# Kernel tuning notes

Hardware: AMD Instinct MI355X
Metric: run time of the kernel (lower is better)

## Reference

```python
import jax, jax.numpy as jnp
import numpy as np
import math

B, S, H, NH = 2, 2048, 2048, 16
HD = H // NH
LAYER_NUMBER = 5
NORM_FACTOR = math.sqrt(HD) * LAYER_NUMBER  # sqrt(head_dim) * coeff
BETA = 1.0 / LAYER_NUMBER
SCALE = float(LAYER_NUMBER)  # ScaledSoftmax scale = coeff
MASK_VALUE = -10000.0


def setup_inputs() -> dict:
    key = jax.random.key(0)
    ks = jax.random.split(key, 6)
    inv_sqrt_h = 1.0 / math.sqrt(H)
    return {
        "hidden_states": jax.random.normal(ks[0], (B, S, H), jnp.float32),
        "alibi": jax.random.normal(ks[1], (NH, 1, S), jnp.float32) * 0.1,
        "w_qkv": jax.random.normal(ks[2], (3 * H, H), jnp.float32) * inv_sqrt_h,
        "b_qkv": jax.random.normal(ks[3], (3 * H,), jnp.float32) * 0.02,
        "w_dense": jax.random.normal(ks[4], (H, H), jnp.float32) * inv_sqrt_h,
        "b_dense": jax.random.normal(ks[5], (H,), jnp.float32) * 0.02,
        "attention_mask": jnp.ones((B, S), jnp.int32),
    }


def reference(hidden_states, alibi, w_qkv, b_qkv, w_dense, b_dense, attention_mask):
    b, s, h = hidden_states.shape
    # QKV projection: [b, s, 3h] -> [b, s, nh, 3*hd] -> split
    mixed = hidden_states @ w_qkv.T + b_qkv
    mixed = mixed.reshape(b, s, NH, 3 * HD)
    q, k, v = jnp.split(mixed, 3, axis=-1)  # each [b, s, nh, hd]

    # Faithful Megatron-style memory reinterpretation (row-major reshape),
    # exactly matching torch's .contiguous().view(s, b*nh, hd).
    q2 = jnp.swapaxes(q.reshape(s, b * NH, HD), 0, 1)  # [b*nh, q_len, hd]
    k2 = jnp.swapaxes(k.reshape(s, b * NH, HD), 0, 1)  # [b*nh, k_len, hd]
    v2 = jnp.swapaxes(v.reshape(s, b * NH, HD), 0, 1)  # [b*nh, k_len, hd]

    # baddbmm: alibi*beta + (q @ k^T)/norm_factor
    alibi_b = jnp.tile(alibi, (b, 1, 1))[: b * NH, :, :s]  # [b*nh, 1, k_len]
    scores = alibi_b * BETA + jnp.einsum("bqd,bkd->bqk", q2, k2) * (1.0 / NORM_FACTOR)
    scores = scores.reshape(b, NH, s, s)

    # ScaledSoftmax: scale then fused causal+padding mask fill, then softmax
    scores = scores * SCALE
    pad_bool = (1 - attention_mask).astype(bool)  # True where padded
    causal = jnp.tril(jnp.ones((s, s), dtype=bool))
    bad = pad_bool[:, None, :, None] | (~causal)[None, None, :, :]  # [b,1,s,s]
    scores = jnp.where(bad, MASK_VALUE, scores)
    probs = jax.nn.softmax(scores, axis=-1)  # [b, nh, s, s]

    # context = probs @ V with the same faithful reshapes
    probs_r = probs.reshape(b * NH, s, s)
    context = jnp.einsum("bqk,bkd->bqd", probs_r, v2)  # [b*nh, q_len, hd]
    context = context.reshape(b, NH, s, HD)
    context = jnp.transpose(context, (2, 0, 1, 3)).reshape(s, b, h)  # [s, b, h]

    out = context @ w_dense.T + b_dense  # [s, b, h]
    return jnp.swapaxes(out, 0, 1)  # [b, s, h]
```

## Files before the change

### kernel.cpp

```cpp
#include <hip/hip_runtime.h>

typedef unsigned short u16;
typedef __bf16  bf16x8 __attribute__((ext_vector_type(8)));
typedef float   f32x4  __attribute__((ext_vector_type(4)));
typedef u16     u16x8  __attribute__((ext_vector_type(8)));
typedef u16     u16x4  __attribute__((ext_vector_type(4)));

#define QSCALE 0.12751744545f

__device__ __forceinline__ u16 f2b(float f) {
    unsigned u = __float_as_uint(f);
    unsigned r = u + 0x7FFFu + ((u >> 16) & 1u);
    return (u16)(r >> 16);
}
__device__ __forceinline__ float b2f(u16 b) {
    return __uint_as_float(((unsigned)b) << 16);
}
__device__ __forceinline__ void async16(const u16* g, u16* l) {
    __builtin_amdgcn_global_load_lds(
        (__attribute__((address_space(1))) void*)(u16*)g,
        (__attribute__((address_space(3))) void*)l, 16, 0, 0);
}

__global__ void cvt_f32_bf16(const float* __restrict__ in, u16* __restrict__ out, int n4) {
    int i = blockIdx.x * blockDim.x + threadIdx.x;
    if (i >= n4) return;
    float4 f = ((const float4*)in)[i];
    u16x4 o;
    o[0] = f2b(f.x); o[1] = f2b(f.y); o[2] = f2b(f.z); o[3] = f2b(f.w);
    *(u16x4*)(out + (size_t)i * 4) = o;
}

__global__ void cvt_wqkv(const float* __restrict__ in, u16* __restrict__ out, int n4) {
    int i = blockIdx.x * blockDim.x + threadIdx.x;
    if (i >= n4) return;
    int row = i >> 9;
    float s = ((row % 384) < 128) ? QSCALE : 1.0f;
    float4 f = ((const float4*)in)[i];
    u16x4 o;
    o[0] = f2b(f.x * s); o[1] = f2b(f.y * s); o[2] = f2b(f.z * s); o[3] = f2b(f.w * s);
    *(u16x4*)(out + (size_t)i * 4) = o;
}

__global__ __launch_bounds__(512, 2) void gemm_qkv(
    const u16* __restrict__ A, const u16* __restrict__ B,
    const float* __restrict__ bias,
    u16* __restrict__ qb, u16* __restrict__ kb, u16* __restrict__ vb)
{
    constexpr int K  = 2048;
    constexpr int NS = K / 32;
    __shared__ u16 lds[65536];

    const int tid = threadIdx.x, wave = tid >> 6, lane = tid & 63;
    const int lm = lane & 15, lg = lane >> 4;
    const int wr = wave >> 2, wc = wave & 3;

    const int rbase = blockIdx.y * 256;
    const int cbase = blockIdx.x * 256;

    const int srl = lane >> 2;
    const int scs = ((lane & 3) ^ ((lane >> 3) & 3)) << 3;
    const u16* sl0;
    int lbase;
    {
        int qq = (wave & 3) * 4;
        if (wave < 4) { sl0 = A + (size_t)rbase * K; lbase = qq * 512; }
        else          { sl0 = B + (size_t)cbase * K; lbase = 8192 + qq * 512; }
        sl0 += (size_t)(qq * 16 + srl) * K + scs;
    }
    auto stage2 = [&](int s_, int c0) {
        int slot = (s_ & 3) * 16384;
        size_t k0 = (size_t)s_ * 32;
        for (int c = c0; c < c0 + 2; c++)
            async16(sl0 + (size_t)c * 16 * K + k0, &lds[slot + lbase + c * 512]);
    };

    const int coff = (lg ^ ((lm >> 1) & 3)) << 3;
    const int aoff = (wr * 128 + lm) * 32 + coff;
    const int boff = 8192 + (wc * 64 + lm) * 32 + coff;

    f32x4 acc[8][4];
    for (int m = 0; m < 8; m++)
        for (int n = 0; n < 4; n++)
            acc[m][n] = (f32x4){0.f, 0.f, 0.f, 0.f};

    stage2(0, 0); stage2(0, 2);
    stage2(1, 0); stage2(1, 2);
    stage2(2, 0); stage2(2, 2);
    asm volatile("s_waitcnt vmcnt(8)" ::: "memory");
    __builtin_amdgcn_s_barrier();

    for (int s = 0; s < NS; s++) {
        const u16* sl = &lds[(s & 3) * 16384];
        bf16x8 af[4], bf[4];

        for (int n = 0; n < 4; n++) bf[n] = *(const bf16x8*)&sl[boff + n * 512];
        for (int m = 0; m < 4; m++) af[m] = *(const bf16x8*)&sl[aoff + m * 512];
        if (s + 3 < NS) stage2(s + 3, 0);
        __builtin_amdgcn_s_barrier();
        __builtin_amdgcn_s_setprio(1);
        for (int m = 0; m < 4; m++)
            for (int n = 0; n < 4; n++)
                acc[m][n] = __builtin_amdgcn_mfma_f32_16x16x32_bf16(af[m], bf[n], acc[m][n], 0, 0, 0);
        __builtin_amdgcn_s_setprio(0);
        __builtin_amdgcn_s_barrier();

        for (int m = 0; m < 4; m++) af[m] = *(const bf16x8*)&sl[aoff + (m + 4) * 512];
        if (s + 3 < NS) stage2(s + 3, 2);
        __builtin_amdgcn_s_barrier();
        __builtin_amdgcn_s_setprio(1);
        for (int m = 0; m < 4; m++)
            for (int n = 0; n < 4; n++)
                acc[m + 4][n] = __builtin_amdgcn_mfma_f32_16x16x32_bf16(af[m], bf[n], acc[m + 4][n], 0, 0, 0);
        __builtin_amdgcn_s_setprio(0);

        if (s + 1 < NS) {
            if (s < NS - 3)       asm volatile("s_waitcnt vmcnt(8)" ::: "memory");
            else if (s == NS - 3) asm volatile("s_waitcnt vmcnt(4)" ::: "memory");
            else                  asm volatile("s_waitcnt vmcnt(0)" ::: "memory");
            __builtin_amdgcn_s_barrier();
        }
    }

    __syncthreads();

    const int ct   = (cbase >> 7) + (wc >> 1);
    const int nh   = ct / 3, part = ct - nh * 3;
    const int hd0  = (wc & 1) * 64;
    const int posb = (rbase >> 11) << 10;
    const int sblk = (rbase & 2047) + wr * 128;

    if (part < 2) {
        u16* dst0 = part ? kb : qb;
        const float bsc = part ? 1.0f : QSCALE;
        for (int n = 0; n < 4; n++) {
            int hd = hd0 + n * 16 + lm;
            float bv = bias[ct * 128 + hd] * bsc;
            for (int m = 0; m < 8; m++) {
                for (int r = 0; r < 4; r++) {
                    int s_  = sblk + m * 16 + lg * 4 + r;
                    int bn  = (s_ & 1) * 16 + nh;
                    int pos = posb + (s_ >> 1);
                    dst0[((size_t)(bn * 2048 + pos)) * 128 + hd] = f2b(acc[m][n][r] + bv);
                }
            }
        }
    } else {
        u16* scr = &lds[wave * 8192];
        for (int n = 0; n < 4; n++) {
            int hdl = n * 16 + lm;
            float bv = bias[ct * 128 + hd0 + hdl];
            for (int m = 0; m < 8; m++)
                for (int r = 0; r < 4; r++)
                    scr[(m * 16 + lg * 4 + r) * 64 + hdl] = f2b(acc[m][n][r] + bv);
        }
        int pos0 = posb + (sblk >> 1);
        for (int par = 0; par < 2; par++) {
            int bn = par * 16 + nh;
            u16* dst = vb + ((size_t)(bn * 128 + hd0 + lane)) * 2048 + pos0;
            for (int p8 = 0; p8 < 8; p8++) {
                u16x8 w;
                for (int e = 0; e < 8; e++)
                    w[e] = scr[(2 * (p8 * 8 + e) + par) * 64 + lane];
                *(u16x8*)(dst + p8 * 8) = w;
            }
        }
    }
}

__global__ __launch_bounds__(256) void gemm_bt(
    const u16* __restrict__ A, const u16* __restrict__ B,
    const float* __restrict__ bias, void* __restrict__ C,
    u16* __restrict__ qb, u16* __restrict__ kb, u16* __restrict__ vb,
    int M, int N, int K, int mode)
{
    __shared__ u16 smem[16384];
    u16* As = smem;
    u16* Bs = smem + 8192;

    int tid = threadIdx.x, wave = tid >> 6, lane = tid & 63;
    int lg = lane >> 4, lm = lane & 15;
    int wm = (wave & 1) * 64, wn = (wave >> 1) * 64;

    const u16* Ab = A + (size_t)(blockIdx.y * 128) * K;
    const u16* Bb = B + (size_t)(blockIdx.x * 128) * K;

    f32x4 acc[4][4];
    for (int i = 0; i < 4; i++)
        for (int j = 0; j < 4; j++)
            acc[i][j] = (f32x4){0.f, 0.f, 0.f, 0.f};

    int srow = (lane >> 2), skq = (lane & 3) * 8;

    for (int k0 = 0; k0 < K; k0 += 64) {
        __syncthreads();
        for (int cc = wave; cc < 16; cc += 4) {
            int p = cc >> 3, c = cc & 7;
            int row = c * 16 + srow;
            size_t off = (size_t)row * K + k0 + p * 32 + skq;
            async16(Ab + off, &As[p * 4096 + c * 512]);
            async16(Bb + off, &Bs[p * 4096 + c * 512]);
        }
        __syncthreads();

        for (int p = 0; p < 2; p++) {
            bf16x8 af[4], bf[4];
            for (int i = 0; i < 4; i++) af[i] = *(const bf16x8*)&As[p * 4096 + (wm + i * 16 + lm) * 32 + lg * 8];
            for (int j = 0; j < 4; j++) bf[j] = *(const bf16x8*)&Bs[p * 4096 + (wn + j * 16 + lm) * 32 + lg * 8];
            for (int i = 0; i < 4; i++)
                for (int j = 0; j < 4; j++)
                    acc[i][j] = __builtin_amdgcn_mfma_f32_16x16x32_bf16(af[i], bf[j], acc[i][j], 0, 0, 0);
        }
    }

    if (mode == 1) {
        for (int j = 0; j < 4; j++) {
            int col = blockIdx.x * 128 + wn + j * 16 + lm;
            float bv = bias[col];
            for (int i = 0; i < 4; i++) {
                int row0 = blockIdx.y * 128 + wm + i * 16 + lg * 4;
                for (int r = 0; r < 4; r++) {
                    int row = row0 + r;
                    int orow = ((row & 1) << 11) + (row >> 1);
                    ((float*)C)[(size_t)orow * N + col] = acc[i][j][r] + bv;
                }
            }
        }
        return;
    }

    int ct = blockIdx.x;
    int nh = ct / 3, part = ct - nh * 3;
    float bscale = (part == 0) ? QSCALE : 1.0f;
    int rbase = blockIdx.y * 128;
    int b = rbase >> 11;
    int s0 = rbase & 2047;

    if (part < 2) {
        u16* dst0 = part ? kb : qb;
        for (int j = 0; j < 4; j++) {
            int hd = wn + j * 16 + lm;
            float bv = bias[ct * 128 + hd] * bscale;
            for (int i = 0; i < 4; i++) {
                for (int r = 0; r < 4; r++) {
                    int rl = wm + i * 16 + lg * 4 + r;
                    int s = s0 + rl;
                    int bn = (s & 1) * 16 + nh;
                    int pos = (b << 10) + (s >> 1);
                    dst0[((size_t)(bn * 2048 + pos)) * 128 + hd] = f2b(acc[i][j][r] + bv);
                }
            }
        }
    } else {
        u16 (*arr)[64][128] = (u16(*)[64][128])smem;
        __syncthreads();
        for (int j = 0; j < 4; j++) {
            int hd = wn + j * 16 + lm;
            float bv = bias[ct * 128 + hd];
            for (int i = 0; i < 4; i++) {
                for (int r = 0; r < 4; r++) {
                    int rl = wm + i * 16 + lg * 4 + r;
                    arr[rl & 1][rl >> 1][hd] = f2b(acc[i][j][r] + bv);
                }
            }
        }
        __syncthreads();
        int hd = tid & 127, par = tid >> 7;
        int bn = par * 16 + nh;
        int pos0 = (b << 10) + (s0 >> 1);
        u16* dst = vb + ((size_t)(bn * 128 + hd)) * 2048 + pos0;
        for (int c = 0; c < 8; c++) {
            u16x8 w;
            for (int e = 0; e < 8; e++) w[e] = arr[par][c * 8 + e][hd];
            *(u16x8*)(dst + c * 8) = w;
        }
    }
}

__global__ __launch_bounds__(256) void attn(
    const u16* __restrict__ qb, const u16* __restrict__ kb,
    const u16* __restrict__ vb, const float* __restrict__ alibi,
    u16* __restrict__ ctx)
{
    __shared__ u16 Ks[64 * 136];
    __shared__ u16 Vt[128 * 88];
    __shared__ u16 Ps[4][16 * 72];

    int bn = blockIdx.y;
    int tid = threadIdx.x, wave = tid >> 6, lane = tid & 63;
    int lg = lane >> 4, lm = lane & 15;

    const float* al = alibi + (bn & 15) * 2048;

    int krow = tid >> 2, kq = (tid & 3) * 32;
    int vhd  = tid >> 1, vh2 = (tid & 1) * 32;
    const u16* ksrc0 = kb + (size_t)(bn * 2048 + krow) * 128 + kq;
    const u16* vsrc0 = vb + (size_t)(bn * 128 + vhd) * 2048 + vh2;

    u16* ps = &Ps[wave][0];
    bf16x8 ones;
    {
        u16x8 t;
        for (int j = 0; j < 8; j++) t[j] = 0x3F80;
        ones = *(bf16x8*)&t;
    }

    for (int pass = 0; pass < 2; pass++) {
        int qt = pass ? (31 - blockIdx.x) : blockIdx.x;
        int q0 = qt * 64;

        bf16x8 qf[4];
        {
            const u16* qp = qb + ((size_t)bn * 2048 + q0 + wave * 16 + lm) * 128 + lg * 8;
            for (int kc = 0; kc < 4; kc++) qf[kc] = *(const bf16x8*)(qp + kc * 32);
        }

        f32x4 o[9];
        for (int i = 0; i < 9; i++) o[i] = (f32x4){0.f, 0.f, 0.f, 0.f};

        u16x8 kreg[4], vreg[4];
        for (int i = 0; i < 4; i++) kreg[i] = *(const u16x8*)(ksrc0 + i * 8);
        for (int i = 0; i < 4; i++) vreg[i] = *(const u16x8*)(vsrc0 + i * 8);

        for (int kt = 0; kt <= qt; kt++) {
            int k0 = kt * 64;
            __syncthreads();
            {
                u16* d1 = &Ks[krow * 136 + kq];
                for (int i = 0; i < 4; i++) *(u16x8*)(d1 + i * 8) = kreg[i];
                u16* d2 = &Vt[vhd * 88 + vh2];
                for (int i = 0; i < 4; i++) *(u16x8*)(d2 + i * 8) = vreg[i];
            }
            __syncthreads();

            if (kt < qt) {
                const u16* s1 = ksrc0 + (size_t)(kt + 1) * 64 * 128;
                const u16* s2 = vsrc0 + (kt + 1) * 64;
                for (int i = 0; i < 4; i++) kreg[i] = *(const u16x8*)(s1 + i * 8);
                for (int i = 0; i < 4; i++) vreg[i] = *(const u16x8*)(s2 + i * 8);
            }

            f32x4 sc[4];
            for (int tc = 0; tc < 4; tc++) {
                const u16* kr = &Ks[(tc * 16 + lm) * 136 + lg * 8];
                f32x4 a = (f32x4){0.f, 0.f, 0.f, 0.f};
                for (int kc = 0; kc < 4; kc++)
                    a = __builtin_amdgcn_mfma_f32_16x16x32_bf16(qf[kc], *(const bf16x8*)(kr + kc * 32), a, 0, 0, 0);
                sc[tc] = a;
            }

            bool diag = (kt == qt);
            for (int tc = 0; tc < 4; tc++) {
                int kg = k0 + tc * 16 + lm;
                float av = (al[kg] - 8.0f) * 1.4426950408889634f;
                for (int r = 0; r < 4; r++) {
                    float v = sc[tc][r] + av;
                    if (diag && kg > q0 + wave * 16 + lg * 4 + r) v = -3e38f;
                    ps[(lg * 4 + r) * 72 + tc * 16 + lm] = f2b(__builtin_amdgcn_exp2f(v));
                }
            }

            for (int kc = 0; kc < 2; kc++) {
                bf16x8 pf = *(const bf16x8*)&ps[lm * 72 + kc * 32 + lg * 8];
                for (int i = 0; i < 8; i++) {
                    bf16x8 vf = *(const bf16x8*)&Vt[(i * 16 + lm) * 88 + kc * 32 + lg * 8];
                    o[i] = __builtin_amdgcn_mfma_f32_16x16x32_bf16(pf, vf, o[i], 0, 0, 0);
                }
                o[8] = __builtin_amdgcn_mfma_f32_16x16x32_bf16(pf, ones, o[8], 0, 0, 0);
            }
        }

        for (int r = 0; r < 4; r++) {
            float inv = 1.0f / o[8][r];
            int qg = q0 + wave * 16 + lg * 4 + r;
            int row = qg * 2 + (bn >> 4);
            u16* crow = ctx + (size_t)row * 2048 + (bn & 15) * 128 + lm;
            for (int i = 0; i < 8; i++)
                crow[i * 16] = f2b(o[i][r] * inv);
        }
    }
}

extern "C" void kernel_launch(void* const* d_in, const int* in_sizes, int n_in,
                              void* d_out, int out_size, void* d_ws, size_t ws_size,
                              hipStream_t stream)
{
    const float* hs    = (const float*)d_in[0];
    const float* alibi = (const float*)d_in[1];
    const float* wqkv  = (const float*)d_in[2];
    const float* bqkv  = (const float*)d_in[3];
    const float* wd    = (const float*)d_in[4];
    const float* bd    = (const float*)d_in[5];
    float* out = (float*)d_out;

    char* ws = (char*)d_ws;
    u16* wqkv_b = (u16*)(ws + 0);
    u16* hs_b   = (u16*)(ws + 25165824);
    u16* ctx    = (u16*)(ws + 41943040);
    u16* wd_b   = wqkv_b;
    u16* qb     = (u16*)(ws + 92274688);
    u16* kb     = (u16*)(ws + 109051904);
    u16* vb     = (u16*)(ws + 125829120);

    cvt_f32_bf16<<<8192,  256, 0, stream>>>(hs,   hs_b,   2097152);
    cvt_wqkv   <<<12288, 256, 0, stream>>>(wqkv, wqkv_b, 3145728);

    gemm_qkv<<<dim3(24, 16), 512, 0, stream>>>(hs_b, wqkv_b, bqkv, qb, kb, vb);

    cvt_f32_bf16<<<4096, 256, 0, stream>>>(wd, wd_b, 1048576);

    attn<<<dim3(16, 32), 256, 0, stream>>>(qb, kb, vb, alibi, ctx);

    gemm_bt<<<dim3(16, 32), 256, 0, stream>>>(ctx, wd_b, bd, out,
                                              nullptr, nullptr, nullptr, 4096, 2048, 2048, 1);
}
```

Before: 403.8 us.

## Enlarge attention query tile to 128 rows with XOR-swizzled LDS layout

Each attention workgroup now handles 128 query rows, with every wave computing two 16-row fragments against each K/V tile loaded into LDS. This halves the grid to 8x32 and doubles reuse of each K/V tile. Row padding in the LDS arrays is replaced by an XOR swizzle to avoid bank conflicts. Waves skip key tiles that lie entirely above their causal diagonal. An unused QKV epilogue in the generic GEMM is also deleted. The trade-off is fewer workgroups and more registers per wave, which may reduce occupancy and latency hiding.

New measurement: 411.6 us. No clear change (+1.9%).

```diff
diff --git a/kernel.cpp b/kernel.cpp
--- a/kernel.cpp
+++ b/kernel.cpp
@@ -228,53 +228,6 @@
         }
         return;
     }
-
-    int ct = blockIdx.x;
-    int nh = ct / 3, part = ct - nh * 3;
-    float bscale = (part == 0) ? QSCALE : 1.0f;
-    int rbase = blockIdx.y * 128;
-    int b = rbase >> 11;
-    int s0 = rbase & 2047;
-
-    if (part < 2) {
-        u16* dst0 = part ? kb : qb;
-        for (int j = 0; j < 4; j++) {
-            int hd = wn + j * 16 + lm;
-            float bv = bias[ct * 128 + hd] * bscale;
-            for (int i = 0; i < 4; i++) {
-                for (int r = 0; r < 4; r++) {
-                    int rl = wm + i * 16 + lg * 4 + r;
-                    int s = s0 + rl;
-                    int bn = (s & 1) * 16 + nh;
-                    int pos = (b << 10) + (s >> 1);
-                    dst0[((size_t)(bn * 2048 + pos)) * 128 + hd] = f2b(acc[i][j][r] + bv);
-                }
-            }
-        }
-    } else {
-        u16 (*arr)[64][128] = (u16(*)[64][128])smem;
-        __syncthreads();
-        for (int j = 0; j < 4; j++) {
-            int hd = wn + j * 16 + lm;
-            float bv = bias[ct * 128 + hd];
-            for (int i = 0; i < 4; i++) {
-                for (int r = 0; r < 4; r++) {
-                    int rl = wm + i * 16 + lg * 4 + r;
-                    arr[rl & 1][rl >> 1][hd] = f2b(acc[i][j][r] + bv);
-                }
-            }
-        }
-        __syncthreads();
-        int hd = tid & 127, par = tid >> 7;
-        int bn = par * 16 + nh;
-        int pos0 = (b << 10) + (s0 >> 1);
-        u16* dst = vb + ((size_t)(bn * 128 + hd)) * 2048 + pos0;
-        for (int c = 0; c < 8; c++) {
-            u16x8 w;
-            for (int e = 0; e < 8; e++) w[e] = arr[par][c * 8 + e][hd];
-            *(u16x8*)(dst + c * 8) = w;
-        }
-    }
 }
 
 __global__ __launch_bounds__(256) void attn(
@@ -282,13 +235,14 @@
     const u16* __restrict__ vb, const float* __restrict__ alibi,
     u16* __restrict__ ctx)
 {
-    __shared__ u16 Ks[64 * 136];
-    __shared__ u16 Vt[128 * 88];
-    __shared__ u16 Ps[4][16 * 72];
+    __shared__ u16 Ks[64 * 128];
+    __shared__ u16 Vt[128 * 64];
+    __shared__ u16 Ps[4][32 * 64];
 
     int bn = blockIdx.y;
     int tid = threadIdx.x, wave = tid >> 6, lane = tid & 63;
     int lg = lane >> 4, lm = lane & 15;
+    const int rxor = (lm & 7) * 8;
 
     const float* al = alibi + (bn & 15) * 2048;
 
@@ -296,6 +250,8 @@
     int vhd  = tid >> 1, vh2 = (tid & 1) * 32;
     const u16* ksrc0 = kb + (size_t)(bn * 2048 + krow) * 128 + kq;
     const u16* vsrc0 = vb + (size_t)(bn * 128 + vhd) * 2048 + vh2;
+    const int kxor = (krow & 7) * 8;
+    const int vxor = (vhd & 7) * 8;
 
     u16* ps = &Ps[wave][0];
     bf16x8 ones;
@@ -306,77 +262,98 @@
     }
 
     for (int pass = 0; pass < 2; pass++) {
-        int qt = pass ? (31 - blockIdx.x) : blockIdx.x;
-        int q0 = qt * 64;
-
-        bf16x8 qf[4];
-        {
-            const u16* qp = qb + ((size_t)bn * 2048 + q0 + wave * 16 + lm) * 128 + lg * 8;
-            for (int kc = 0; kc < 4; kc++) qf[kc] = *(const bf16x8*)(qp + kc * 32);
-        }
-
-        f32x4 o[9];
-        for (int i = 0; i < 9; i++) o[i] = (f32x4){0.f, 0.f, 0.f, 0.f};
+        int qtb = pass ? (15 - blockIdx.x) : blockIdx.x;
+        int q0 = qtb * 128;
+        int ktmax = 2 * qtb + 1;
+        int qrow0 = q0 + wave * 32;
+
+        bf16x8 qf[2][4];
+        for (int f = 0; f < 2; f++) {
+            const u16* qp = qb + ((size_t)bn * 2048 + qrow0 + f * 16 + lm) * 128 + lg * 8;
+            for (int kc = 0; kc < 4; kc++) qf[f][kc] = *(const bf16x8*)(qp + kc * 32);
+        }
+
+        f32x4 o[2][9];
+        for (int f = 0; f < 2; f++)
+            for (int i = 0; i < 9; i++) o[f][i] = (f32x4){0.f, 0.f, 0.f, 0.f};
 
         u16x8 kreg[4], vreg[4];
         for (int i = 0; i < 4; i++) kreg[i] = *(const u16x8*)(ksrc0 + i * 8);
         for (int i = 0; i < 4; i++) vreg[i] = *(const u16x8*)(vsrc0 + i * 8);
 
-        for (int kt = 0; kt <= qt; kt++) {
+        for (int kt = 0; kt <= ktmax; kt++) {
             int k0 = kt * 64;
             __syncthreads();
             {
-                u16* d1 = &Ks[krow * 136 + kq];
-                for (int i = 0; i < 4; i++) *(u16x8*)(d1 + i * 8) = kreg[i];
-                u16* d2 = &Vt[vhd * 88 + vh2];
-                for (int i = 0; i < 4; i++) *(u16x8*)(d2 + i * 8) = vreg[i];
+                u16* d1 = &Ks[krow * 128];
+                for (int i = 0; i < 4; i++) *(u16x8*)&d1[(kq + i * 8) ^ kxor] = kreg[i];
+                u16* d2 = &Vt[vhd * 64];
+                for (int i = 0; i < 4; i++) *(u16x8*)&d2[(vh2 + i * 8) ^ vxor] = vreg[i];
             }
             __syncthreads();
 
-            if (kt < qt) {
+            if (kt < ktmax) {
                 const u16* s1 = ksrc0 + (size_t)(kt + 1) * 64 * 128;
                 const u16* s2 = vsrc0 + (kt + 1) * 64;
                 for (int i = 0; i < 4; i++) kreg[i] = *(const u16x8*)(s1 + i * 8);
                 for (int i = 0; i < 4; i++) vreg[i] = *(const u16x8*)(s2 + i * 8);
             }
 
-            f32x4 sc[4];
-            for (int tc = 0; tc < 4; tc++) {
-                const u16* kr = &Ks[(tc * 16 + lm) * 136 + lg * 8];
-                f32x4 a = (f32x4){0.f, 0.f, 0.f, 0.f};
-                for (int kc = 0; kc < 4; kc++)
-                    a = __builtin_amdgcn_mfma_f32_16x16x32_bf16(qf[kc], *(const bf16x8*)(kr + kc * 32), a, 0, 0, 0);
-                sc[tc] = a;
-            }
-
-            bool diag = (kt == qt);
-            for (int tc = 0; tc < 4; tc++) {
-                int kg = k0 + tc * 16 + lm;
-                float av = (al[kg] - 8.0f) * 1.4426950408889634f;
-                for (int r = 0; r < 4; r++) {
-                    float v = sc[tc][r] + av;
-                    if (diag && kg > q0 + wave * 16 + lg * 4 + r) v = -3e38f;
-                    ps[(lg * 4 + r) * 72 + tc * 16 + lm] = f2b(__builtin_amdgcn_exp2f(v));
-                }
-            }
-
-            for (int kc = 0; kc < 2; kc++) {
-                bf16x8 pf = *(const bf16x8*)&ps[lm * 72 + kc * 32 + lg * 8];
-                for (int i = 0; i < 8; i++) {
-                    bf16x8 vf = *(const bf16x8*)&Vt[(i * 16 + lm) * 88 + kc * 32 + lg * 8];
-                    o[i] = __builtin_amdgcn_mfma_f32_16x16x32_bf16(pf, vf, o[i], 0, 0, 0);
-                }
-                o[8] = __builtin_amdgcn_mfma_f32_16x16x32_bf16(pf, ones, o[8], 0, 0, 0);
-            }
-        }
-
-        for (int r = 0; r < 4; r++) {
-            float inv = 1.0f / o[8][r];
-            int qg = q0 + wave * 16 + lg * 4 + r;
-            int row = qg * 2 + (bn >> 4);
-            u16* crow = ctx + (size_t)row * 2048 + (bn & 15) * 128 + lm;
-            for (int i = 0; i < 8; i++)
-                crow[i * 16] = f2b(o[i][r] * inv);
+            bool act = (k0 <= qrow0 + 31);
+            if (act) {
+                f32x4 sc[2][4];
+                for (int tc = 0; tc < 4; tc++) {
+                    const u16* kr = &Ks[(tc * 16 + lm) * 128];
+                    bf16x8 krf[4];
+                    for (int kc = 0; kc < 4; kc++)
+                        krf[kc] = *(const bf16x8*)&kr[(kc * 32 + lg * 8) ^ rxor];
+                    for (int f = 0; f < 2; f++) {
+                        f32x4 a = (f32x4){0.f, 0.f, 0.f, 0.f};
+                        for (int kc = 0; kc < 4; kc++)
+                            a = __builtin_amdgcn_mfma_f32_16x16x32_bf16(qf[f][kc], krf[kc], a, 0, 0, 0);
+                        sc[f][tc] = a;
+                    }
+                }
+
+                bool dz = (kt >= 2 * qtb);
+                for (int tc = 0; tc < 4; tc++) {
+                    int kg = k0 + tc * 16 + lm;
+                    float av = (al[kg] - 8.0f) * 1.4426950408889634f;
+                    for (int f = 0; f < 2; f++) {
+                        for (int r = 0; r < 4; r++) {
+                            float v = sc[f][tc][r] + av;
+                            if (dz && kg > qrow0 + f * 16 + lg * 4 + r) v = -3e38f;
+                            int row = f * 16 + lg * 4 + r;
+                            ps[row * 64 + ((tc * 16 + lm) ^ ((row & 7) * 8))] =
+                                f2b(__builtin_amdgcn_exp2f(v));
+                        }
+                    }
+                }
+
+                for (int kc = 0; kc < 2; kc++) {
+                    bf16x8 pf[2];
+                    for (int f = 0; f < 2; f++)
+                        pf[f] = *(const bf16x8*)&ps[(f * 16 + lm) * 64 + ((kc * 32 + lg * 8) ^ rxor)];
+                    for (int i = 0; i < 8; i++) {
+                        bf16x8 vf = *(const bf16x8*)&Vt[(i * 16 + lm) * 64 + ((kc * 32 + lg * 8) ^ rxor)];
+                        for (int f = 0; f < 2; f++)
+                            o[f][i] = __builtin_amdgcn_mfma_f32_16x16x32_bf16(pf[f], vf, o[f][i], 0, 0, 0);
+                    }
+                    for (int f = 0; f < 2; f++)
+                        o[f][8] = __builtin_amdgcn_mfma_f32_16x16x32_bf16(pf[f], ones, o[f][8], 0, 0, 0);
+                }
+            }
+        }
+
+        for (int f = 0; f < 2; f++) {
+            for (int r = 0; r < 4; r++) {
+                float inv = 1.0f / o[f][8][r];
+                int qg = qrow0 + f * 16 + lg * 4 + r;
+                int row = qg * 2 + (bn >> 4);
+                u16* crow = ctx + (size_t)row * 2048 + (bn & 15) * 128 + lm;
+                for (int i = 0; i < 8; i++)
+                    crow[i * 16] = f2b(o[f][i][r] * inv);
+            }
         }
     }
 }
@@ -409,7 +386,7 @@
 
     cvt_f32_bf16<<<4096, 256, 0, stream>>>(wd, wd_b, 1048576);
 
-    attn<<<dim3(16, 32), 256, 0, stream>>>(qb, kb, vb, alibi, ctx);
+    attn<<<dim3(8, 32), 256, 0, stream>>>(qb, kb, vb, alibi, ctx);
 
     gemm_bt<<<dim3(16, 32), 256, 0, stream>>>(ctx, wd_b, bd, out,
                                               nullptr, nullptr, nullptr, 4096, 2048, 2048, 1);
```
